# Kernel tuning notes

Measured on AMD Instinct MI355X. Metric: run time of the kernel, lower is better.

Reference implementation:

```python
import jax, jax.numpy as jnp
import numpy as np

E = 768   # embed_dim
S = 128   # slots
T = 3     # recurrence steps
B = 64    # batch
L = 512   # sequence length of z
LN_EPS = 1e-5


def _layernorm(x, g, b):
    mu = jnp.mean(x, axis=-1, keepdims=True)
    var = jnp.mean((x - mu) ** 2, axis=-1, keepdims=True)
    return (x - mu) / jnp.sqrt(var + LN_EPS) * g + b


def _mha(q, k, v, Wq, bq, Wk, bk, Wv, bv, Wo, bo):
    # single-head MultiheadAttention, batch_first; PyTorch Linear: x @ W.T + b
    Q = q @ Wq.T + bq                     # [B, Lq, E]
    K = k @ Wk.T + bk                     # [B, Lk, E]
    V = v @ Wv.T + bv
    scale = 1.0 / jnp.sqrt(jnp.asarray(Q.shape[-1], Q.dtype))
    scores = jnp.einsum('bqe,bke->bqk', Q, K) * scale
    A = jax.nn.softmax(scores, axis=-1)
    O = jnp.einsum('bqk,bke->bqe', A, V)
    return O @ Wo.T + bo


def _gru_cell(x, h, Wih, bih, Whh, bhh):
    # PyTorch GRUCell gate order: r, z, n
    gi = x @ Wih.T + bih
    gh = h @ Whh.T + bhh
    i_r, i_z, i_n = jnp.split(gi, 3, axis=-1)
    h_r, h_z, h_n = jnp.split(gh, 3, axis=-1)
    r = jax.nn.sigmoid(i_r + h_r)
    zt = jax.nn.sigmoid(i_z + h_z)
    n = jnp.tanh(i_n + r * h_n)
    return (1.0 - zt) * n + zt * h


def setup_inputs() -> dict:
    key = jax.random.key(0)
    ks = jax.random.split(key, 24)
    w = lambda k, shape: jax.random.normal(k, shape, dtype=jnp.float32) * 0.02
    inp = {
        'z': jax.random.normal(ks[0], (B, L, E), dtype=jnp.float32),
        'slots': w(ks[1], (1, S, E)),
        'ln_g': jnp.ones((E,), jnp.float32),
        'ln_b': jnp.zeros((E,), jnp.float32),
        # write attention
        'w_wq': w(ks[2], (E, E)), 'w_bq': jnp.zeros((E,), jnp.float32),
        'w_wk': w(ks[3], (E, E)), 'w_bk': jnp.zeros((E,), jnp.float32),
        'w_wv': w(ks[4], (E, E)), 'w_bv': jnp.zeros((E,), jnp.float32),
        'w_wo': w(ks[5], (E, E)), 'w_bo': jnp.zeros((E,), jnp.float32),
        # read attention
        'r_wq': w(ks[6], (E, E)), 'r_bq': jnp.zeros((E,), jnp.float32),
        'r_wk': w(ks[7], (E, E)), 'r_bk': jnp.zeros((E,), jnp.float32),
        'r_wv': w(ks[8], (E, E)), 'r_bv': jnp.zeros((E,), jnp.float32),
        'r_wo': w(ks[9], (E, E)), 'r_bo': jnp.zeros((E,), jnp.float32),
        # GRUCell
        'gru_wih': w(ks[10], (3 * E, E)), 'gru_bih': jnp.zeros((3 * E,), jnp.float32),
        'gru_whh': w(ks[11], (3 * E, E)), 'gru_bhh': jnp.zeros((3 * E,), jnp.float32),
    }
    return inp


def reference(z, slots, ln_g, ln_b,
              w_wq, w_bq, w_wk, w_bk, w_wv, w_bv, w_wo, w_bo,
              r_wq, r_bq, r_wk, r_bk, r_wv, r_bv, r_wo, r_bo,
              gru_wih, gru_bih, gru_whh, gru_bhh):
    bsz = z.shape[0]
    memory = jnp.broadcast_to(slots, (bsz, S, E))
    for _ in range(T):
        memory = _layernorm(memory, ln_g, ln_b)
        upd = _mha(memory, z, z, w_wq, w_bq, w_wk, w_bk, w_wv, w_bv, w_wo, w_bo)
        memory = _gru_cell(upd.reshape(-1, E), memory.reshape(-1, E),
                           gru_wih, gru_bih, gru_whh, gru_bhh).reshape(bsz, S, E)
    out = _mha(z, memory, memory, r_wq, r_bq, r_wk, r_bk, r_wv, r_bv, r_wo, r_bo)
    return out
```

## Files before the change

### kernel.cpp

```cpp
#include <hip/hip_runtime.h>
#include <hip/hip_bf16.h>
#include <math.h>


typedef __attribute__((ext_vector_type(4))) float f32x4;
typedef __attribute__((ext_vector_type(8))) short short8;
typedef __attribute__((ext_vector_type(4))) unsigned short us4;

__device__ __forceinline__ unsigned short f2bf(float x) {
  union { float f; unsigned u; } v; v.f = x;
  unsigned r = v.u + 0x7fffu + ((v.u >> 16) & 1u);
  return (unsigned short)(r >> 16);
}
__device__ __forceinline__ float bf2f(unsigned short u) {
  union { unsigned u; float f; } v; v.u = (unsigned)u << 16; return v.f;
}

__device__ __forceinline__ void g2l16(const void* g, void* l) {
  __builtin_amdgcn_global_load_lds(
      (const __attribute__((address_space(1))) unsigned int*)g,
      (__attribute__((address_space(3))) unsigned int*)l, 16, 0, 0);
}

__device__ __forceinline__ float wsum(float v) {
#pragma unroll
  for (int o = 32; o > 0; o >>= 1) v += __shfl_xor(v, o, 64);
  return v;
}
__device__ __forceinline__ float wmax(float v) {
#pragma unroll
  for (int o = 32; o > 0; o >>= 1) v = fmaxf(v, __shfl_xor(v, o, 64));
  return v;
}

__device__ __forceinline__ void xcd_map(int& tn, int& tm, long long& bz) {
  const int gx = gridDim.x, gy = gridDim.y, gz = gridDim.z;
  const int nwg = gx * gy * gz;
  const int lin = blockIdx.x + gx * (blockIdx.y + gy * blockIdx.z);
  const int q = nwg >> 3, r = nwg & 7;
  const int xcd = lin & 7, jj = lin >> 3;
  const int w = (xcd < r ? xcd * (q + 1) : r * (q + 1) + (xcd - r) * q) + jj;
  tn = w % gx;
  const int t2 = w / gx;
  tm = t2 % gy;
  bz = t2 / gy;
}

__device__ __forceinline__ void c_write_128(
    void* Cg, size_t cb, int N, int tm, int tn, int wr, int wc, int lane,
    const f32x4 acc[4][4], const float* bias, bool has_bias, float alpha, int omode)
{
#pragma unroll
  for (int a = 0; a < 4; ++a) {
    const int row0 = tm * 128 + wr * 64 + a * 16 + (lane >> 4) * 4;
#pragma unroll
    for (int b = 0; b < 4; ++b) {
      const int col = tn * 128 + wc * 64 + b * 16 + (lane & 15);
      float bv = has_bias ? bias[col] : 0.f;
#pragma unroll
      for (int rr = 0; rr < 4; ++rr) {
        float v = acc[a][b][rr] * alpha + bv;
        if (omode == 0)
          ((float*)Cg)[cb + (size_t)(row0 + rr) * N + col] = v;
        else
          ((unsigned short*)Cg)[cb + (size_t)(row0 + rr) * N + col] = f2bf(v);
      }
    }
  }
}

template<int OMODE, bool BIAS>
__device__ __forceinline__ void gemm_body(
    const unsigned short* __restrict__ A, const unsigned short* __restrict__ B,
    const float* __restrict__ bias, void* __restrict__ Cg, size_t cb,
    int N, int K, int tm, int tn, float alpha,
    unsigned short* As, unsigned short* Bs)
{
  const int tid  = threadIdx.x;
  const int lane = tid & 63;
  const int wv   = tid >> 6;
  const int wr   = wv >> 1, wc = wv & 1;

  A += (size_t)tm * 128 * K;
  B += (size_t)tn * 128 * K;

  const int srow = wv * 16 + (lane >> 2);
  const int kby  = (lane & 3) * 16;

  f32x4 acc[4][4];
#pragma unroll
  for (int a = 0; a < 4; ++a)
#pragma unroll
    for (int b = 0; b < 4; ++b) acc[a][b] = (f32x4)(0.f);

  const int mrow = wr * 64 + (lane & 15);
  const int nrow = wc * 64 + (lane & 15);
  const int koff = (lane >> 4) * 8;

  for (int kt = 0; kt < K; kt += 32) {
#pragma unroll
    for (int i = 0; i < 2; ++i) {
      g2l16((const char*)(A + (size_t)(i * 64 + srow) * K + kt) + kby,
            (char*)As + i * 4096 + wv * 1024);
      g2l16((const char*)(B + (size_t)(i * 64 + srow) * K + kt) + kby,
            (char*)Bs + i * 4096 + wv * 1024);
    }
    __syncthreads();
    short8 af[4], bf[4];
#pragma unroll
    for (int a = 0; a < 4; ++a) af[a] = *(const short8*)&As[(mrow + a * 16) * 32 + koff];
#pragma unroll
    for (int b = 0; b < 4; ++b) bf[b] = *(const short8*)&Bs[(nrow + b * 16) * 32 + koff];
#pragma unroll
    for (int a = 0; a < 4; ++a)
#pragma unroll
      for (int b = 0; b < 4; ++b)
        acc[a][b] = __builtin_amdgcn_mfma_f32_16x16x32_bf16(af[a], bf[b], acc[a][b], 0, 0, 0);
    __syncthreads();
  }
  c_write_128(Cg, cb, N, tm, tn, wr, wc, lane, acc, bias, BIAS, alpha, OMODE);
}

template<int OMODE, bool BIAS>
__global__ __launch_bounds__(256) void gemm_nt(
    const unsigned short* __restrict__ Ag, const unsigned short* __restrict__ Bg,
    const float* __restrict__ bias, void* __restrict__ Cg,
    int M, int N, int K, long long sA, long long sB, long long sC,
    long long sBias, float alpha)
{
  __shared__ __align__(16) unsigned short As[128 * 32];
  __shared__ __align__(16) unsigned short Bs[128 * 32];
  int tn, tm; long long bz;
  xcd_map(tn, tm, bz);
  const float* bp = BIAS ? bias + bz * sBias : (const float*)nullptr;
  gemm_body<OMODE, BIAS>(Ag + bz * sA, Bg + bz * sB, bp, Cg,
                         (size_t)(bz * sC), N, K, tm, tn, alpha, As, Bs);
}

template<int OMODE, bool BIAS>
__global__ __launch_bounds__(256) void gemm_nt64(
    const unsigned short* __restrict__ Ag, const unsigned short* __restrict__ Bg,
    const float* __restrict__ bias, void* __restrict__ Cg,
    int M, int N, int K, long long sA, long long sB, long long sC,
    long long sBias, float alpha)
{
  __shared__ __align__(16) unsigned short As[128 * 64];
  __shared__ __align__(16) unsigned short Bs[128 * 64];

  const int tid  = threadIdx.x;
  const int lane = tid & 63;
  const int wv   = tid >> 6;
  const int wr   = wv >> 1, wc = wv & 1;

  int tn, tm; long long bz;
  xcd_map(tn, tm, bz);

  const unsigned short* A = Ag + bz * sA + (size_t)tm * 128 * K;
  const unsigned short* B = Bg + bz * sB + (size_t)tn * 128 * K;

  auto swz = [](int o) { return o ^ (((o >> 7) & 7) << 4); };
  int srow[4], scb[4];
#pragma unroll
  for (int c = 0; c < 4; ++c) {
    const int olog = swz(c * 4096 + tid * 16);
    srow[c] = olog >> 7;
    scb[c]  = olog & 127;
  }

  f32x4 acc[4][4];
#pragma unroll
  for (int a = 0; a < 4; ++a)
#pragma unroll
    for (int b = 0; b < 4; ++b) acc[a][b] = (f32x4)(0.f);

  const int mrow = wr * 64 + (lane & 15);
  const int nrow = wc * 64 + (lane & 15);
  const int kb   = (lane >> 4) * 16;

  for (int kt = 0; kt < K; kt += 64) {
#pragma unroll
    for (int c = 0; c < 4; ++c) {
      g2l16((const char*)(A + (size_t)srow[c] * K + kt) + scb[c],
            (char*)As + c * 4096 + wv * 1024);
      g2l16((const char*)(B + (size_t)srow[c] * K + kt) + scb[c],
            (char*)Bs + c * 4096 + wv * 1024);
    }
    __syncthreads();
#pragma unroll
    for (int h = 0; h < 2; ++h) {
      short8 af[4], bf[4];
#pragma unroll
      for (int a = 0; a < 4; ++a)
        af[a] = *(const short8*)((char*)As + swz((mrow + a * 16) * 128 + h * 64 + kb));
#pragma unroll
      for (int b = 0; b < 4; ++b)
        bf[b] = *(const short8*)((char*)Bs + swz((nrow + b * 16) * 128 + h * 64 + kb));
#pragma unroll
      for (int a = 0; a < 4; ++a)
#pragma unroll
        for (int b = 0; b < 4; ++b)
          acc[a][b] = __builtin_amdgcn_mfma_f32_16x16x32_bf16(af[a], bf[b], acc[a][b], 0, 0, 0);
    }
    __syncthreads();
  }

  const float* bp = BIAS ? bias + bz * sBias : (const float*)nullptr;
  c_write_128(Cg, (size_t)(bz * sC), N, tm, tn, wr, wc, lane, acc, bp, BIAS, alpha, OMODE);
}

struct QuadPtrs {
  const unsigned short* a[4];
  const unsigned short* b[4];
  unsigned short* c[4];
};
__global__ __launch_bounds__(256) void gemm_nt_quad(QuadPtrs p) {
  __shared__ __align__(16) unsigned short As[128 * 32];
  __shared__ __align__(16) unsigned short Bs[128 * 32];
  const int zi = blockIdx.z;
  gemm_body<1, false>(p.a[zi], p.b[zi], nullptr, (void*)p.c[zi], 0,
                      768, 768, blockIdx.y, blockIdx.x, 1.0f, As, Bs);
}

template<int LR>
__global__ __launch_bounds__(256) void softmax_kernel(
    const float* __restrict__ sc, unsigned short* __restrict__ p)
{
  const int row  = blockIdx.x * 4 + (threadIdx.x >> 6);
  const int lane = threadIdx.x & 63;
  constexpr int PER = LR / 64;
  const float* sr = sc + (size_t)row * LR;
  float v[PER];
  float m = -1e30f;
#pragma unroll
  for (int j = 0; j < PER; ++j) { v[j] = sr[lane + 64 * j]; m = fmaxf(m, v[j]); }
  m = wmax(m);
  float s = 0.f;
#pragma unroll
  for (int j = 0; j < PER; ++j) { v[j] = __expf(v[j] - m); s += v[j]; }
  s = wsum(s);
  const float inv = 1.f / s;
  unsigned short* pr = p + (size_t)row * LR;
#pragma unroll
  for (int j = 0; j < PER; ++j) pr[lane + 64 * j] = f2bf(v[j] * inv);
}

template<bool GHB, bool EMITLN>
__global__ __launch_bounds__(256) void gru_ln_combine(
    const unsigned short* __restrict__ gi, const unsigned short* __restrict__ gh,
    float* __restrict__ mem, const float* __restrict__ g, const float* __restrict__ b,
    unsigned short* __restrict__ outb)
{
  __shared__ float ps[4], pq[4];
  const size_t row = blockIdx.x;
  const int tid = threadIdx.x, wv = tid >> 6, lane = tid & 63;
  float* mr = mem + row * 768;
  const size_t ghrow = GHB ? (row & 127) : row;
  float v[3];
  float s = 0.f, q = 0.f;
#pragma unroll
  for (int k = 0; k < 3; ++k) {
    v[k] = mr[tid + 256 * k];
    s += v[k]; q += v[k] * v[k];
  }
  s = wsum(s); q = wsum(q);
  if (lane == 0) { ps[wv] = s; pq[wv] = q; }
  __syncthreads();
  s = ps[0] + ps[1] + ps[2] + ps[3];
  q = pq[0] + pq[1] + pq[2] + pq[3];
  const float mu = s * (1.f / 768.f);
  const float rstd = rsqrtf(q * (1.f / 768.f) - mu * mu + 1e-5f);
  float nv[3];
  float s2 = 0.f, q2 = 0.f;
#pragma unroll
  for (int k = 0; k < 3; ++k) {
    const int c = tid + 256 * k;
    const float h = (v[k] - mu) * rstd * g[c] + b[c];
    const float ir  = bf2f(gi[row * 2304 + c]);
    const float iz  = bf2f(gi[row * 2304 + 768 + c]);
    const float in_ = bf2f(gi[row * 2304 + 1536 + c]);
    const float hr  = bf2f(gh[ghrow * 2304 + c]);
    const float hz  = bf2f(gh[ghrow * 2304 + 768 + c]);
    const float hn  = bf2f(gh[ghrow * 2304 + 1536 + c]);
    const float rg = 1.f / (1.f + __expf(-(ir + hr)));
    const float zg = 1.f / (1.f + __expf(-(iz + hz)));
    const float n  = tanhf(in_ + rg * hn);
    nv[k] = (1.f - zg) * n + zg * h;
    mr[c] = nv[k];
    s2 += nv[k]; q2 += nv[k] * nv[k];
  }
  if (EMITLN) {
    s2 = wsum(s2); q2 = wsum(q2);
    __syncthreads();
    if (lane == 0) { ps[wv] = s2; pq[wv] = q2; }
    __syncthreads();
    s2 = ps[0] + ps[1] + ps[2] + ps[3];
    q2 = pq[0] + pq[1] + pq[2] + pq[3];
    const float mu2 = s2 * (1.f / 768.f);
    const float rstd2 = rsqrtf(q2 * (1.f / 768.f) - mu2 * mu2 + 1e-5f);
#pragma unroll
    for (int k = 0; k < 3; ++k) {
      const int c = tid + 256 * k;
      outb[row * 768 + c] = f2bf((nv[k] - mu2) * rstd2 * g[c] + b[c]);
    }
  } else {
#pragma unroll
    for (int k = 0; k < 3; ++k) {
      const int c = tid + 256 * k;
      outb[row * 768 + c] = f2bf(nv[k]);
    }
  }
}

__global__ __launch_bounds__(256) void cvt_weights(
    const float* p0, const float* p1, const float* p2, const float* p3,
    const float* p4, const float* p5, const float* p6, const float* p7,
    const float* p8, const float* p9, unsigned short* __restrict__ dst)
{
  const int i = blockIdx.x * 256 + threadIdx.x;
  if (i >= 2064384) return;
  const float* src; int base;
  if      (i < 147456)  { src = p0; base = 0; }
  else if (i < 294912)  { src = p1; base = 147456; }
  else if (i < 442368)  { src = p2; base = 294912; }
  else if (i < 589824)  { src = p3; base = 442368; }
  else if (i < 737280)  { src = p4; base = 589824; }
  else if (i < 884736)  { src = p5; base = 737280; }
  else if (i < 1032192) { src = p6; base = 884736; }
  else if (i < 1179648) { src = p7; base = 1032192; }
  else if (i < 1622016) { src = p8; base = 1179648; }
  else                  { src = p9; base = 1622016; }
  const float4 v = ((const float4*)src)[i - base];
  us4 o;
  o.x = f2bf(v.x); o.y = f2bf(v.y); o.z = f2bf(v.z); o.w = f2bf(v.w);
  ((us4*)dst)[i] = o;
}

__global__ __launch_bounds__(256) void init_mem(
    const float* __restrict__ slots, const float* __restrict__ g,
    const float* __restrict__ b, float* __restrict__ memf,
    unsigned short* __restrict__ memb)
{
  __shared__ float ps[4], pq[4];
  const int s = blockIdx.x;
  const int tid = threadIdx.x, wv = tid >> 6, lane = tid & 63;
  const float* sr = slots + (size_t)s * 768;
  float v[3];
  float su = 0.f, qu = 0.f;
#pragma unroll
  for (int k = 0; k < 3; ++k) { v[k] = sr[tid + 256 * k]; su += v[k]; qu += v[k] * v[k]; }
  su = wsum(su); qu = wsum(qu);
  if (lane == 0) { ps[wv] = su; pq[wv] = qu; }
  __syncthreads();
  su = ps[0] + ps[1] + ps[2] + ps[3];
  qu = pq[0] + pq[1] + pq[2] + pq[3];
  const float mu = su * (1.f / 768.f);
  const float rstd = rsqrtf(qu * (1.f / 768.f) - mu * mu + 1e-5f);
  unsigned short lb[3];
#pragma unroll
  for (int k = 0; k < 3; ++k) {
    const int c = tid + 256 * k;
    lb[k] = f2bf((v[k] - mu) * rstd * g[c] + b[c]);
  }
  for (int bb = 0; bb < 64; ++bb) {
    float* mrow = memf + ((size_t)bb * 128 + s) * 768;
    unsigned short* brow = memb + ((size_t)bb * 128 + s) * 768;
#pragma unroll
    for (int k = 0; k < 3; ++k) { mrow[tid + 256 * k] = v[k]; brow[tid + 256 * k] = lb[k]; }
  }
}

struct TPtrs { const unsigned short* s[6]; unsigned short* d[6]; };
__global__ void transpose_multi(TPtrs p) {
  __shared__ unsigned short t[32][33];
  const unsigned short* in = p.s[blockIdx.z];
  unsigned short* out = p.d[blockIdx.z];
  const int c0 = blockIdx.x * 32, r0 = blockIdx.y * 32;
  const int x = threadIdx.x, y = threadIdx.y;
#pragma unroll
  for (int k = 0; k < 32; k += 8)
    t[y + k][x] = in[(size_t)(r0 + y + k) * 768 + c0 + x];
  __syncthreads();
#pragma unroll
  for (int k = 0; k < 32; k += 8)
    out[(size_t)(c0 + y + k) * 768 + r0 + x] = t[x][y + k];
}

__global__ __launch_bounds__(256) void matvec_T2(
    const float* __restrict__ W0, const float* __restrict__ x0, float* __restrict__ y0,
    const float* __restrict__ W1, const float* __restrict__ x1, float* __restrict__ y1)
{
  const int task = blockIdx.x / 3;
  const int j = (blockIdx.x % 3) * 256 + threadIdx.x;
  const float* W = task ? W1 : W0;
  const float* x = task ? x1 : x0;
  float* y = task ? y1 : y0;
  float s = 0.f;
  for (int k = 0; k < 768; ++k) s += W[(size_t)k * 768 + j] * x[k];
  y[j] = s;
}

__global__ __launch_bounds__(256) void matvec_row2(
    const float* __restrict__ W0, const float* __restrict__ x0,
    const float* __restrict__ a0, float* __restrict__ y0,
    const float* __restrict__ W1, const float* __restrict__ x1,
    const float* __restrict__ a1, float* __restrict__ y1)
{
  const int task = blockIdx.x / 192;
  const int row = (blockIdx.x % 192) * 4 + (threadIdx.x >> 6);
  const int lane = threadIdx.x & 63;
  const float* W = task ? W1 : W0;
  const float* x = task ? x1 : x0;
  const float* ad = task ? a1 : a0;
  float* y = task ? y1 : y0;
  const float* r = W + (size_t)row * 768;
  float s = 0.f;
#pragma unroll
  for (int j = 0; j < 12; ++j) s += r[lane + 64 * j] * x[lane + 64 * j];
  s = wsum(s);
  if (lane == 0) y[row] = s + ad[row];
}

__global__ __launch_bounds__(256) void rowdot768(
    const float* __restrict__ src, const float* __restrict__ vec,
    const float* __restrict__ cadd, float* __restrict__ out, float scl, int rows)
{
  const int row  = blockIdx.x * 4 + (threadIdx.x >> 6);
  if (row >= rows) return;
  const int lane = threadIdx.x & 63;
  const float* r = src + (size_t)row * 768;
  float s = 0.f;
#pragma unroll
  for (int j = 0; j < 12; ++j) s += r[lane + 64 * j] * vec[lane + 64 * j];
  s = wsum(s);
  if (lane == 0) out[row] = scl * (s + (cadd ? cadd[0] : 0.f));
}

__global__ __launch_bounds__(256) void cvt_z_zv(
    const float* __restrict__ z, unsigned short* __restrict__ zb,
    const float* __restrict__ vw, const float* __restrict__ cw,
    float* __restrict__ zv, float scl)
{
  const int row = blockIdx.x * 4 + (threadIdx.x >> 6);
  const int lane = threadIdx.x & 63;
  const float* zr = z + (size_t)row * 768;
  unsigned short* zbr = zb + (size_t)row * 768;
  float s = 0.f;
#pragma unroll
  for (int j = 0; j < 12; ++j) {
    const float v = zr[lane + 64 * j];
    s += v * vw[lane + 64 * j];
    zbr[lane + 64 * j] = f2bf(v);
  }
  s = wsum(s);
  if (lane == 0) zv[row] = scl * (s + cw[0]);
}

__global__ __launch_bounds__(256) void diag_ws(float* __restrict__ out, float wsz, int n) {
  const int i = blockIdx.x * 256 + threadIdx.x;
  if (i < n) out[i] = (i == 0) ? wsz : 0.f;
}

extern "C" void kernel_launch(void* const* d_in, const int* in_sizes, int n_in,
                              void* d_out, int out_size, void* d_ws, size_t ws_size,
                              hipStream_t stream)
{
  const float* z     = (const float*)d_in[0];
  const float* slots = (const float*)d_in[1];
  const float* ln_g  = (const float*)d_in[2];
  const float* ln_b  = (const float*)d_in[3];
  const float* w_wq = (const float*)d_in[4];  const float* w_bq = (const float*)d_in[5];
  const float* w_wk = (const float*)d_in[6];  const float* w_bk = (const float*)d_in[7];
  const float* w_wv = (const float*)d_in[8];  const float* w_bv = (const float*)d_in[9];
  const float* w_wo = (const float*)d_in[10]; const float* w_bo = (const float*)d_in[11];
  const float* r_wq = (const float*)d_in[12]; const float* r_bq = (const float*)d_in[13];
  const float* r_wk = (const float*)d_in[14]; const float* r_bk = (const float*)d_in[15];
  const float* r_wv = (const float*)d_in[16]; const float* r_bv = (const float*)d_in[17];
  const float* r_wo = (const float*)d_in[18]; const float* r_bo = (const float*)d_in[19];
  const float* g_wih = (const float*)d_in[20]; const float* g_bih = (const float*)d_in[21];
  const float* g_whh = (const float*)d_in[22]; const float* g_bhh = (const float*)d_in[23];

  constexpr size_t O_F    = 16515072;
  constexpr size_t O_T6   = 21233664;
  constexpr size_t O_GH0  = 28311552;
  constexpr size_t O_FL   = 28901376;
  constexpr size_t O_memf = 29096192;
  constexpr size_t O_Kz   = 54262016;
  constexpr size_t O_VwoT = 104593664;
  constexpr size_t O_L    = 154925312;
  constexpr size_t NEED   = 217839872;

  if (ws_size < NEED) {
    hipLaunchKernelGGL(diag_ws, dim3((out_size + 255) / 256), dim3(256), 0, stream,
                       (float*)d_out, (float)ws_size, out_size);
    return;
  }

  char* ws = (char*)d_ws;
  unsigned short* wqb  = (unsigned short*)(ws + 0);
  unsigned short* wkb  = wqb + 589824;
  unsigned short* wvb  = wkb + 589824;
  unsigned short* wob  = wvb + 589824;
  unsigned short* rqb  = wob + 589824;
  unsigned short* rkb  = rqb + 589824;
  unsigned short* rvb  = rkb + 589824;
  unsigned short* rob  = rvb + 589824;
  unsigned short* wihb = rob + 589824;
  unsigned short* whhb = wihb + 1769472;
  unsigned short* Fqk  = (unsigned short*)(ws + O_F);
  unsigned short* Fwv  = Fqk + 589824;
  unsigned short* Fvo  = Fwv + 589824;
  unsigned short* Frq  = Fvo + 589824;
  unsigned short* T0   = (unsigned short*)(ws + O_T6);
  unsigned short* T1   = T0 + 589824;
  unsigned short* T2   = T1 + 589824;
  unsigned short* T3   = T2 + 589824;
  unsigned short* T4   = T3 + 589824;
  unsigned short* T5   = T4 + 589824;
  unsigned short* gh0  = (unsigned short*)(ws + O_GH0);
  float* bih_c   = (float*)(ws + O_FL);
  float* bhh_c   = bih_c + 2304;
  float* const_o = bhh_c + 2304;
  float* bvo     = const_o + 768;
  float* vw      = bvo + 768;
  float* vr      = vw + 768;
  float* cw      = vr + 768;
  float* zv      = cw + 64;
  float* colb    = zv + 32768;
  float* memf = (float*)(ws + O_memf);
  unsigned short* Kz    = (unsigned short*)(ws + O_Kz);
  unsigned short* memFr = (unsigned short*)(ws + O_Kz);
  unsigned short* VwoT  = (unsigned short*)(ws + O_VwoT);
  unsigned short* memVoT  = (unsigned short*)(ws + O_VwoT);
  float*          Sbr     = (float*)(ws + O_VwoT + 25165824);
  unsigned short* Abr     = (unsigned short*)(ws + O_VwoT + 41943040);
  char* L = ws + O_L;
  unsigned short* memb  = (unsigned short*)(L + 0);
  unsigned short* updb  = (unsigned short*)(L + 12582912);
  float*          Sbuf  = (float*)(L + 25165824);
  unsigned short* Abuf  = (unsigned short*)(L + 41943040);
  unsigned short* gib   = (unsigned short*)(L + 25165824);
  unsigned short* ghb   = (unsigned short*)d_out;
  unsigned short* zb    = (unsigned short*)((char*)d_out + 50331648);

  const float scale = 1.0f / sqrtf(768.f);

  hipLaunchKernelGGL(cvt_weights, dim3(8064), dim3(256), 0, stream,
      w_wq, w_wk, w_wv, w_wo, r_wq, r_wk, r_wv, r_wo, g_wih, g_whh, wqb);
  hipMemcpyAsync(bih_c, g_bih, 2304 * 4, hipMemcpyDeviceToDevice, stream);
  hipMemcpyAsync(bhh_c, g_bhh, 2304 * 4, hipMemcpyDeviceToDevice, stream);

  {
    TPtrs tp;
    tp.s[0] = wqb; tp.d[0] = T0;
    tp.s[1] = wkb; tp.d[1] = T1;
    tp.s[2] = wvb; tp.d[2] = T2;
    tp.s[3] = rvb; tp.d[3] = T3;
    tp.s[4] = rqb; tp.d[4] = T4;
    tp.s[5] = rkb; tp.d[5] = T5;
    hipLaunchKernelGGL(transpose_multi, dim3(24, 24, 6), dim3(32, 8), 0, stream, tp);
  }
  {
    QuadPtrs qp;
    qp.a[0] = T0;  qp.b[0] = T1; qp.c[0] = Fqk;
    qp.a[1] = wob; qp.b[1] = T2; qp.c[1] = Fwv;
    qp.a[2] = rob; qp.b[2] = T3; qp.c[2] = Fvo;
    qp.a[3] = T4;  qp.b[3] = T5; qp.c[3] = Frq;
    hipLaunchKernelGGL(gemm_nt_quad, dim3(6, 6, 4), dim3(256), 0, stream, qp);
  }

  hipLaunchKernelGGL(matvec_T2, dim3(6), dim3(256), 0, stream,
      w_wk, w_bq, vw, r_wk, r_bq, vr);
  hipLaunchKernelGGL(matvec_row2, dim3(384), dim3(256), 0, stream,
      w_wo, w_bv, w_bo, const_o, r_wo, r_bv, r_bo, bvo);
  hipLaunchKernelGGL(rowdot768, dim3(1), dim3(256), 0, stream,
      w_bq, w_bk, (const float*)nullptr, cw, 1.0f, 1);
  hipLaunchKernelGGL(cvt_z_zv, dim3(8192), dim3(256), 0, stream, z, zb, vw, cw, zv, scale);
  hipLaunchKernelGGL(init_mem, dim3(128), dim3(256), 0, stream,
      slots, ln_g, ln_b, memf, memb);

  hipLaunchKernelGGL((gemm_nt64<1, false>), dim3(4, 6, 64), dim3(256), 0, stream,
      Fwv, zb, (const float*)nullptr, (void*)VwoT, 768, 512, 768,
      0ll, 393216ll, 393216ll, 0ll, 1.0f);
  hipLaunchKernelGGL((gemm_nt64<1, false>), dim3(6, 256, 1), dim3(256), 0, stream,
      zb, Fqk, (const float*)nullptr, (void*)Kz, 32768, 768, 768, 0ll, 0ll, 0ll, 0ll, 1.0f);

  const long long sA_g = (long long)(memb - updb);
  const long long sC_g = (long long)(ghb - gib);

  for (int t = 0; t < 3; ++t) {
    hipLaunchKernelGGL((gemm_nt<0, true>), dim3(4, 1, 64), dim3(256), 0, stream,
        memb, Kz, zv, (void*)Sbuf, 128, 512, 768,
        98304ll, 393216ll, 65536ll, 512ll, scale);
    hipLaunchKernelGGL((softmax_kernel<512>), dim3(2048), dim3(256), 0, stream, Sbuf, Abuf);
    hipLaunchKernelGGL((gemm_nt<1, true>), dim3(6, 1, 64), dim3(256), 0, stream,
        Abuf, VwoT, const_o, (void*)updb, 128, 768, 512,
        65536ll, 393216ll, 98304ll, 0ll, 1.0f);
    if (t == 0) {
      hipLaunchKernelGGL((gemm_nt64<1, true>), dim3(18, 1, 1), dim3(256), 0, stream,
          memb, whhb, bhh_c, (void*)gh0, 128, 2304, 768, 0ll, 0ll, 0ll, 0ll, 1.0f);
      hipLaunchKernelGGL((gemm_nt64<1, true>), dim3(18, 64, 1), dim3(256), 0, stream,
          updb, wihb, bih_c, (void*)gib, 8192, 2304, 768, 0ll, 0ll, 0ll, 0ll, 1.0f);
      hipLaunchKernelGGL((gru_ln_combine<true, true>), dim3(8192), dim3(256), 0, stream,
          gib, gh0, memf, ln_g, ln_b, memb);
    } else {
      hipLaunchKernelGGL((gemm_nt64<1, true>), dim3(18, 64, 2), dim3(256), 0, stream,
          updb, wihb, bih_c, (void*)gib, 8192, 2304, 768,
          sA_g, 1769472ll, sC_g, 2304ll, 1.0f);
      if (t < 2)
        hipLaunchKernelGGL((gru_ln_combine<false, true>), dim3(8192), dim3(256), 0, stream,
            gib, ghb, memf, ln_g, ln_b, memb);
      else
        hipLaunchKernelGGL((gru_ln_combine<false, false>), dim3(8192), dim3(256), 0, stream,
            gib, ghb, memf, ln_g, ln_b, memb);
    }
  }

  hipLaunchKernelGGL((gemm_nt64<1, false>), dim3(6, 64, 1), dim3(256), 0, stream,
      memb, Frq, (const float*)nullptr, (void*)memFr, 8192, 768, 768,
      0ll, 0ll, 0ll, 0ll, 1.0f);
  hipLaunchKernelGGL((gemm_nt64<1, false>), dim3(1, 6, 64), dim3(256), 0, stream,
      Fvo, memb, (const float*)nullptr, (void*)memVoT, 768, 128, 768,
      0ll, 98304ll, 98304ll, 0ll, 1.0f);
  hipLaunchKernelGGL(rowdot768, dim3(2048), dim3(256), 0, stream,
      memf, vr, (const float*)nullptr, colb, scale, 8192);
  hipLaunchKernelGGL((gemm_nt<0, true>), dim3(1, 4, 64), dim3(256), 0, stream,
      zb, memFr, colb, (void*)Sbr, 512, 128, 768,
      393216ll, 98304ll, 65536ll, 128ll, scale);
  hipLaunchKernelGGL((softmax_kernel<128>), dim3(8192), dim3(256), 0, stream, Sbr, Abr);
  hipLaunchKernelGGL((gemm_nt<0, true>), dim3(6, 4, 64), dim3(256), 0, stream,
      Abr, memVoT, bvo, d_out, 512, 768, 128,
      65536ll, 98304ll, 393216ll, 0ll, 1.0f);
}
```

Baseline: 751.0 us.

## Route batched GEMMs through K64 kernel, vectorize softmax/matvec, parallelize init_mem

All remaining gemm_nt launches (attention scores, A·V, final read attention) now use the gemm_nt64 kernel with a 64-wide K tile instead of a 32-wide one, which halves the number of K-loop iterations and barriers. The softmax over 512 columns, matvec_row2, rowdot768 and the z conversion kernel now use float4 loads and 4-wide bf16 stores instead of scalar accesses. init_mem is split across 8 batch groups, giving 1024 blocks instead of 128 serial 64-batch loops. The K64 tile doubles LDS per block, which may lower occupancy, and it assumes K is a multiple of 64 (true for 768, 512 and 128).

```diff
diff --git a/kernel.cpp b/kernel.cpp
--- a/kernel.cpp
+++ b/kernel.cpp
@@ -122,22 +122,6 @@
 }
 
 template<int OMODE, bool BIAS>
-__global__ __launch_bounds__(256) void gemm_nt(
-    const unsigned short* __restrict__ Ag, const unsigned short* __restrict__ Bg,
-    const float* __restrict__ bias, void* __restrict__ Cg,
-    int M, int N, int K, long long sA, long long sB, long long sC,
-    long long sBias, float alpha)
-{
-  __shared__ __align__(16) unsigned short As[128 * 32];
-  __shared__ __align__(16) unsigned short Bs[128 * 32];
-  int tn, tm; long long bz;
-  xcd_map(tn, tm, bz);
-  const float* bp = BIAS ? bias + bz * sBias : (const float*)nullptr;
-  gemm_body<OMODE, BIAS>(Ag + bz * sA, Bg + bz * sB, bp, Cg,
-                         (size_t)(bz * sC), N, K, tm, tn, alpha, As, Bs);
-}
-
-template<int OMODE, bool BIAS>
 __global__ __launch_bounds__(256) void gemm_nt64(
     const unsigned short* __restrict__ Ag, const unsigned short* __restrict__ Bg,
     const float* __restrict__ bias, void* __restrict__ Cg,
@@ -221,27 +205,58 @@
                       768, 768, blockIdx.y, blockIdx.x, 1.0f, As, Bs);
 }
 
-template<int LR>
-__global__ __launch_bounds__(256) void softmax_kernel(
+__global__ __launch_bounds__(256) void softmax512(
     const float* __restrict__ sc, unsigned short* __restrict__ p)
 {
   const int row  = blockIdx.x * 4 + (threadIdx.x >> 6);
   const int lane = threadIdx.x & 63;
-  constexpr int PER = LR / 64;
-  const float* sr = sc + (size_t)row * LR;
-  float v[PER];
+  const float4* sr = (const float4*)(sc + (size_t)row * 512);
+  float4 v[2];
   float m = -1e30f;
 #pragma unroll
-  for (int j = 0; j < PER; ++j) { v[j] = sr[lane + 64 * j]; m = fmaxf(m, v[j]); }
+  for (int j = 0; j < 2; ++j) {
+    v[j] = sr[lane + 64 * j];
+    m = fmaxf(m, fmaxf(fmaxf(v[j].x, v[j].y), fmaxf(v[j].z, v[j].w)));
+  }
   m = wmax(m);
   float s = 0.f;
 #pragma unroll
-  for (int j = 0; j < PER; ++j) { v[j] = __expf(v[j] - m); s += v[j]; }
+  for (int j = 0; j < 2; ++j) {
+    v[j].x = __expf(v[j].x - m); v[j].y = __expf(v[j].y - m);
+    v[j].z = __expf(v[j].z - m); v[j].w = __expf(v[j].w - m);
+    s += v[j].x + v[j].y + v[j].z + v[j].w;
+  }
   s = wsum(s);
   const float inv = 1.f / s;
-  unsigned short* pr = p + (size_t)row * LR;
-#pragma unroll
-  for (int j = 0; j < PER; ++j) pr[lane + 64 * j] = f2bf(v[j] * inv);
+  us4* pr = (us4*)(p + (size_t)row * 512);
+#pragma unroll
+  for (int j = 0; j < 2; ++j) {
+    us4 o;
+    o.x = f2bf(v[j].x * inv); o.y = f2bf(v[j].y * inv);
+    o.z = f2bf(v[j].z * inv); o.w = f2bf(v[j].w * inv);
+    pr[lane + 64 * j] = o;
+  }
+}
+
+__global__ __launch_bounds__(256) void softmax128(
+    const float* __restrict__ sc, unsigned short* __restrict__ p)
+{
+  const int row  = blockIdx.x * 4 + (threadIdx.x >> 6);
+  const int lane = threadIdx.x & 63;
+  const float* sr = sc + (size_t)row * 128;
+  float v[2];
+  float m = -1e30f;
+#pragma unroll
+  for (int j = 0; j < 2; ++j) { v[j] = sr[lane + 64 * j]; m = fmaxf(m, v[j]); }
+  m = wmax(m);
+  float s = 0.f;
+#pragma unroll
+  for (int j = 0; j < 2; ++j) { v[j] = __expf(v[j] - m); s += v[j]; }
+  s = wsum(s);
+  const float inv = 1.f / s;
+  unsigned short* pr = p + (size_t)row * 128;
+#pragma unroll
+  for (int j = 0; j < 2; ++j) pr[lane + 64 * j] = f2bf(v[j] * inv);
 }
 
 template<bool GHB, bool EMITLN>
@@ -342,6 +357,7 @@
 {
   __shared__ float ps[4], pq[4];
   const int s = blockIdx.x;
+  const int g0 = blockIdx.y * 8;
   const int tid = threadIdx.x, wv = tid >> 6, lane = tid & 63;
   const float* sr = slots + (size_t)s * 768;
   float v[3];
@@ -361,7 +377,7 @@
     const int c = tid + 256 * k;
     lb[k] = f2bf((v[k] - mu) * rstd * g[c] + b[c]);
   }
-  for (int bb = 0; bb < 64; ++bb) {
+  for (int bb = g0; bb < g0 + 8; ++bb) {
     float* mrow = memf + ((size_t)bb * 128 + s) * 768;
     unsigned short* brow = memb + ((size_t)bb * 128 + s) * 768;
 #pragma unroll
@@ -412,10 +428,14 @@
   const float* x = task ? x1 : x0;
   const float* ad = task ? a1 : a0;
   float* y = task ? y1 : y0;
-  const float* r = W + (size_t)row * 768;
+  const float4* r = (const float4*)(W + (size_t)row * 768);
+  const float4* xv = (const float4*)x;
   float s = 0.f;
 #pragma unroll
-  for (int j = 0; j < 12; ++j) s += r[lane + 64 * j] * x[lane + 64 * j];
+  for (int j = 0; j < 3; ++j) {
+    const float4 a = r[lane + 64 * j], c = xv[lane + 64 * j];
+    s += a.x * c.x + a.y * c.y + a.z * c.z + a.w * c.w;
+  }
   s = wsum(s);
   if (lane == 0) y[row] = s + ad[row];
 }
@@ -427,10 +447,14 @@
   const int row  = blockIdx.x * 4 + (threadIdx.x >> 6);
   if (row >= rows) return;
   const int lane = threadIdx.x & 63;
-  const float* r = src + (size_t)row * 768;
+  const float4* r = (const float4*)(src + (size_t)row * 768);
+  const float4* vv = (const float4*)vec;
   float s = 0.f;
 #pragma unroll
-  for (int j = 0; j < 12; ++j) s += r[lane + 64 * j] * vec[lane + 64 * j];
+  for (int j = 0; j < 3; ++j) {
+    const float4 a = r[lane + 64 * j], c = vv[lane + 64 * j];
+    s += a.x * c.x + a.y * c.y + a.z * c.z + a.w * c.w;
+  }
   s = wsum(s);
   if (lane == 0) out[row] = scl * (s + (cadd ? cadd[0] : 0.f));
 }
@@ -442,14 +466,18 @@
 {
   const int row = blockIdx.x * 4 + (threadIdx.x >> 6);
   const int lane = threadIdx.x & 63;
-  const float* zr = z + (size_t)row * 768;
-  unsigned short* zbr = zb + (size_t)row * 768;
+  const float4* zr = (const float4*)(z + (size_t)row * 768);
+  const float4* wv = (const float4*)vw;
+  us4* zbr = (us4*)(zb + (size_t)row * 768);
   float s = 0.f;
 #pragma unroll
-  for (int j = 0; j < 12; ++j) {
-    const float v = zr[lane + 64 * j];
-    s += v * vw[lane + 64 * j];
-    zbr[lane + 64 * j] = f2bf(v);
+  for (int j = 0; j < 3; ++j) {
+    const float4 v = zr[lane + 64 * j];
+    const float4 w = wv[lane + 64 * j];
+    s += v.x * w.x + v.y * w.y + v.z * w.z + v.w * w.w;
+    us4 o;
+    o.x = f2bf(v.x); o.y = f2bf(v.y); o.z = f2bf(v.z); o.w = f2bf(v.w);
+    zbr[lane + 64 * j] = o;
   }
   s = wsum(s);
   if (lane == 0) zv[row] = scl * (s + cw[0]);
@@ -575,7 +603,7 @@
   hipLaunchKernelGGL(rowdot768, dim3(1), dim3(256), 0, stream,
       w_bq, w_bk, (const float*)nullptr, cw, 1.0f, 1);
   hipLaunchKernelGGL(cvt_z_zv, dim3(8192), dim3(256), 0, stream, z, zb, vw, cw, zv, scale);
-  hipLaunchKernelGGL(init_mem, dim3(128), dim3(256), 0, stream,
+  hipLaunchKernelGGL(init_mem, dim3(128, 8), dim3(256), 0, stream,
       slots, ln_g, ln_b, memf, memb);
 
   hipLaunchKernelGGL((gemm_nt64<1, false>), dim3(4, 6, 64), dim3(256), 0, stream,
@@ -588,11 +616,11 @@
   const long long sC_g = (long long)(ghb - gib);
 
   for (int t = 0; t < 3; ++t) {
-    hipLaunchKernelGGL((gemm_nt<0, true>), dim3(4, 1, 64), dim3(256), 0, stream,
+    hipLaunchKernelGGL((gemm_nt64<0, true>), dim3(4, 1, 64), dim3(256), 0, stream,
         memb, Kz, zv, (void*)Sbuf, 128, 512, 768,
         98304ll, 393216ll, 65536ll, 512ll, scale);
-    hipLaunchKernelGGL((softmax_kernel<512>), dim3(2048), dim3(256), 0, stream, Sbuf, Abuf);
-    hipLaunchKernelGGL((gemm_nt<1, true>), dim3(6, 1, 64), dim3(256), 0, stream,
+    hipLaunchKernelGGL(softmax512, dim3(2048), dim3(256), 0, stream, Sbuf, Abuf);
+    hipLaunchKernelGGL((gemm_nt64<1, true>), dim3(6, 1, 64), dim3(256), 0, stream,
         Abuf, VwoT, const_o, (void*)updb, 128, 768, 512,
         65536ll, 393216ll, 98304ll, 0ll, 1.0f);
     if (t == 0) {
@@ -623,11 +651,11 @@
       0ll, 98304ll, 98304ll, 0ll, 1.0f);
   hipLaunchKernelGGL(rowdot768, dim3(2048), dim3(256), 0, stream,
       memf, vr, (const float*)nullptr, colb, scale, 8192);
-  hipLaunchKernelGGL((gemm_nt<0, true>), dim3(1, 4, 64), dim3(256), 0, stream,
+  hipLaunchKernelGGL((gemm_nt64<0, true>), dim3(1, 4, 64), dim3(256), 0, stream,
       zb, memFr, colb, (void*)Sbr, 512, 128, 768,
       393216ll, 98304ll, 65536ll, 128ll, scale);
-  hipLaunchKernelGGL((softmax_kernel<128>), dim3(8192), dim3(256), 0, stream, Sbr, Abr);
-  hipLaunchKernelGGL((gemm_nt<0, true>), dim3(6, 4, 64), dim3(256), 0, stream,
+  hipLaunchKernelGGL(softmax128, dim3(8192), dim3(256), 0, stream, Sbr, Abr);
+  hipLaunchKernelGGL((gemm_nt64<0, true>), dim3(6, 4, 64), dim3(256), 0, stream,
       Abr, memVoT, bvo, d_out, 512, 768, 128,
       65536ll, 98304ll, 393216ll, 0ll, 1.0f);
 }
```

Result: no change. 738.1 us (-1.7%).
